# Performance work log

Measured on AMD Instinct MI355X. Metric: run time of the kernel, lower is better.

Reference implementation:

```python
import jax, jax.numpy as jnp
import numpy as np

B, P, L, M, L_EVAL = 8, 16, 256, 16, 2048
T_MAX = 100.0


def setup_inputs() -> dict:
    key = jax.random.key(0)
    k1, k2, k3, k4, k5 = jax.random.split(key, 5)
    # sorted event times per path (Hawkes event streams are ordered)
    event_times = jnp.sort(jax.random.uniform(k1, (B, P, L), dtype=jnp.float32) * T_MAX, axis=-1)
    # parameters are assumed already positive (post-softplus) -> uniform [0,1)
    mu = jax.random.uniform(k2, (B, M, P, L), dtype=jnp.float32)
    alpha = jax.random.uniform(k3, (B, M, P, L), dtype=jnp.float32)
    beta = jax.random.uniform(k4, (B, M, P, L), dtype=jnp.float32)
    query_times = jax.random.uniform(k5, (B, P, L_EVAL), dtype=jnp.float32) * T_MAX
    return {"query_times": query_times, "event_times": event_times,
            "mu": mu, "alpha": alpha, "beta": beta}


def reference(query_times, event_times, mu, alpha, beta):
    # query_times: [B,P,Le]; event_times: [B,P,L]; mu/alpha/beta: [B,M,P,L]
    b, m, p, l = mu.shape
    le = query_times.shape[-1]
    # index of latest event strictly before each query time (mask + max, as original)
    past_mask = event_times[:, :, None, :] < query_times[:, :, :, None]  # [B,P,Le,L]
    idx = jnp.arange(l, dtype=jnp.int32)
    last_idx = jnp.max(jnp.where(past_mask, idx, -1), axis=-1)            # [B,P,Le]
    ci = jnp.clip(last_idx, 0, None)
    gi = jnp.broadcast_to(ci[:, None, :, :], (b, m, p, le))
    mu_last = jnp.take_along_axis(mu, gi, axis=3)
    alpha_last = jnp.take_along_axis(alpha, gi, axis=3)
    beta_last = jnp.take_along_axis(beta, gi, axis=3)
    t_last = jnp.take_along_axis(event_times, ci, axis=2)                 # [B,P,Le]
    t_last = jnp.where(last_idx == -1, jnp.zeros_like(t_last), t_last)
    delta_t = (query_times - t_last)[:, None, :, :]                       # [B,1,P,Le]
    base = mu_last + (alpha_last - mu_last) * jnp.exp(-beta_last * delta_t)
    return jax.nn.softplus(base)                                          # [B,M,P,Le]
```

## Files before the change

### kernel.cpp

```cpp
#include <hip/hip_runtime.h>

#define BB  8
#define PP  16
#define LL  256
#define MM  16
#define LE  2048
#define THREADS 512
#define TILE THREADS

__device__ __forceinline__ void acc4(const float4 v, const float q, int& cin, float& tl)
{
    bool c;
    c = (v.x < q); cin += c; tl = c ? fmaxf(tl, v.x) : tl;
    c = (v.y < q); cin += c; tl = c ? fmaxf(tl, v.y) : tl;
    c = (v.z < q); cin += c; tl = c ? fmaxf(tl, v.z) : tl;
    c = (v.w < q); cin += c; tl = c ? fmaxf(tl, v.w) : tl;
}

__global__ __launch_bounds__(THREADS, 4) void hawkes_intensity_kernel(
    const float* __restrict__ qt,
    const float* __restrict__ ev,
    const float* __restrict__ mu,
    const float* __restrict__ alpha,
    const float* __restrict__ beta,
    float* __restrict__ out)
{
    __shared__ float2 pma_s[MM * LL];
    __shared__ float  pnb_s[MM * LL];
    __shared__ __align__(16) float ev_s[LL];

    const int tiles_per_bp = LE / TILE;
    const int bp   = blockIdx.x / tiles_per_bp;
    const int tile = blockIdx.x % tiles_per_bp;
    const int b = bp / PP;
    const int p = bp % PP;
    const int t = threadIdx.x;

    const int le = tile * TILE + t;
    const float q = qt[bp * LE + le];

    if (t < LL) ev_s[t] = ev[bp * LL + t];

    #pragma unroll
    for (int i = t; i < MM * LL; i += THREADS) {
        const int m = i >> 8;
        const int l = i & (LL - 1);
        const int g = ((b * MM + m) * PP + p) * LL + l;
        const float mm = mu[g];
        const float aa = alpha[g];
        const float bb = beta[g];
        pma_s[i] = make_float2(mm, aa - mm);
        pnb_s[i] = -bb;
    }
    __syncthreads();

    int F = 0;
    float tl = 0.0f;
    #pragma unroll
    for (int j = 0; j < 16; ++j) {
        const float r = ev_s[j * 16 + 15];
        const bool c = (r < q);
        F += c;
        tl = c ? fmaxf(tl, r) : tl;
    }
    const int Fc = (F < 16) ? F : 15;

    const float4* ev4 = (const float4*)ev_s;
    const float4 w0 = ev4[Fc * 4 + 0];
    const float4 w1 = ev4[Fc * 4 + 1];
    const float4 w2 = ev4[Fc * 4 + 2];
    const float4 w3 = ev4[Fc * 4 + 3];
    int cin = 0;
    acc4(w0, q, cin, tl);
    acc4(w1, q, cin, tl);
    acc4(w2, q, cin, tl);
    acc4(w3, q, cin, tl);

    const int cnt = Fc * 16 + cin;
    const int ci  = (cnt > 0) ? (cnt - 1) : 0;
    const float dt = q - tl;

    int o = (b * MM * PP + p) * LE + le;
    #pragma unroll
    for (int m = 0; m < MM; ++m) {
        const float2 pm = pma_s[(m << 8) | ci];
        const float  nb = pnb_s[(m << 8) | ci];
        const float  e  = __expf(nb * dt);
        const float  base = fmaf(pm.y, e, pm.x);
        out[o] = __logf(1.0f + __expf(base));
        o += PP * LE;
    }
}

extern "C" void kernel_launch(void* const* d_in, const int* in_sizes, int n_in,
                              void* d_out, int out_size, void* d_ws, size_t ws_size,
                              hipStream_t stream) {
    const float* qt    = (const float*)d_in[0];
    const float* ev    = (const float*)d_in[1];
    const float* mu    = (const float*)d_in[2];
    const float* alpha = (const float*)d_in[3];
    const float* beta  = (const float*)d_in[4];
    float* out = (float*)d_out;

    const int nblocks = (BB * PP) * (LE / TILE);
    hawkes_intensity_kernel<<<nblocks, THREADS, 0, stream>>>(qt, ev, mu, alpha, beta, out);
}
```

Measured before the change: 78.32 us.

## Split work by mark groups instead of query tiles to cut redundant parameter loads

The grid now covers (b,p) pairs times groups of two marks, so each block loads only two marks' worth of mu/alpha/beta into shared memory and handles all 2048 queries, four per thread. Before, every query tile reloaded all 16 marks' parameters, which duplicated global reads four times over. The cost is that the event search for each query now repeats across the 8 mark groups. The change also vectorises the parameter loads with float4, swizzles the block index, and raises the launch-bounds occupancy hint.

```diff
diff --git a/kernel.cpp b/kernel.cpp
--- a/kernel.cpp
+++ b/kernel.cpp
@@ -5,8 +5,10 @@
 #define LL  256
 #define MM  16
 #define LE  2048
+#define MG  2
+#define NMG (MM/MG)
 #define THREADS 512
-#define TILE THREADS
+#define QPT (LE/THREADS)
 
 __device__ __forceinline__ void acc4(const float4 v, const float q, int& cin, float& tl)
 {
@@ -17,7 +19,7 @@
     c = (v.w < q); cin += c; tl = c ? fmaxf(tl, v.w) : tl;
 }
 
-__global__ __launch_bounds__(THREADS, 4) void hawkes_intensity_kernel(
+__global__ __launch_bounds__(THREADS, 6) void hawkes_intensity_kernel(
     const float* __restrict__ qt,
     const float* __restrict__ ev,
     const float* __restrict__ mu,
@@ -25,70 +27,88 @@
     const float* __restrict__ beta,
     float* __restrict__ out)
 {
-    __shared__ float2 pma_s[MM * LL];
-    __shared__ float  pnb_s[MM * LL];
+    __shared__ float2 pma_s[MG * LL];
+    __shared__ float  pnb_s[MG * LL];
     __shared__ __align__(16) float ev_s[LL];
 
-    const int tiles_per_bp = LE / TILE;
-    const int bp   = blockIdx.x / tiles_per_bp;
-    const int tile = blockIdx.x % tiles_per_bp;
+    const int lid = (blockIdx.x & 7) * (BB * PP * NMG / 8) + (blockIdx.x >> 3);
+    const int bp  = lid >> 3;
+    const int mg  = lid & (NMG - 1);
     const int b = bp / PP;
     const int p = bp % PP;
     const int t = threadIdx.x;
 
-    const int le = tile * TILE + t;
-    const float q = qt[bp * LE + le];
+    const float* qrow = qt + bp * LE;
+    float qv[QPT];
+    #pragma unroll
+    for (int k = 0; k < QPT; ++k) qv[k] = qrow[k * THREADS + t];
 
-    if (t < LL) ev_s[t] = ev[bp * LL + t];
+    if (t >= 256) ev_s[t - 256] = ev[bp * LL + (t - 256)];
 
-    #pragma unroll
-    for (int i = t; i < MM * LL; i += THREADS) {
-        const int m = i >> 8;
-        const int l = i & (LL - 1);
-        const int g = ((b * MM + m) * PP + p) * LL + l;
-        const float mm = mu[g];
-        const float aa = alpha[g];
-        const float bb = beta[g];
-        pma_s[i] = make_float2(mm, aa - mm);
-        pnb_s[i] = -bb;
+    if (t < (MG * LL / 4)) {
+        const float4* mu4 = (const float4*)mu;
+        const float4* al4 = (const float4*)alpha;
+        const float4* be4 = (const float4*)beta;
+        const int m  = t >> 6;
+        const int l4 = t & 63;
+        const int g  = ((b * MM + mg * MG + m) * PP + p) * (LL / 4) + l4;
+        const float4 mv = mu4[g];
+        const float4 av = al4[g];
+        const float4 bv = be4[g];
+        const float ma[4] = {mv.x, mv.y, mv.z, mv.w};
+        const float aa[4] = {av.x, av.y, av.z, av.w};
+        const float ba[4] = {bv.x, bv.y, bv.z, bv.w};
+        #pragma unroll
+        for (int j = 0; j < 4; ++j) {
+            const int l = (l4 << 2) | j;
+            pma_s[(m << 8) | l] = make_float2(ma[j], aa[j] - ma[j]);
+            pnb_s[(m << 8) | l] = -ba[j];
+        }
     }
     __syncthreads();
 
-    int F = 0;
-    float tl = 0.0f;
+    const float4* ev4 = (const float4*)ev_s;
+
     #pragma unroll
-    for (int j = 0; j < 16; ++j) {
-        const float r = ev_s[j * 16 + 15];
-        const bool c = (r < q);
-        F += c;
-        tl = c ? fmaxf(tl, r) : tl;
-    }
-    const int Fc = (F < 16) ? F : 15;
+    for (int k = 0; k < QPT; ++k) {
+        const int le = k * THREADS + t;
+        const float q = qv[k];
 
-    const float4* ev4 = (const float4*)ev_s;
-    const float4 w0 = ev4[Fc * 4 + 0];
-    const float4 w1 = ev4[Fc * 4 + 1];
-    const float4 w2 = ev4[Fc * 4 + 2];
-    const float4 w3 = ev4[Fc * 4 + 3];
-    int cin = 0;
-    acc4(w0, q, cin, tl);
-    acc4(w1, q, cin, tl);
-    acc4(w2, q, cin, tl);
-    acc4(w3, q, cin, tl);
+        int F = 0;
+        float tl = 0.0f;
+        #pragma unroll
+        for (int j = 0; j < 16; ++j) {
+            const float r = ev_s[j * 16 + 15];
+            const bool c = (r < q);
+            F += c;
+            tl = c ? fmaxf(tl, r) : tl;
+        }
+        const int Fc = (F < 16) ? F : 15;
 
-    const int cnt = Fc * 16 + cin;
-    const int ci  = (cnt > 0) ? (cnt - 1) : 0;
-    const float dt = q - tl;
+        const float4 w0 = ev4[Fc * 4 + 0];
+        const float4 w1 = ev4[Fc * 4 + 1];
+        const float4 w2 = ev4[Fc * 4 + 2];
+        const float4 w3 = ev4[Fc * 4 + 3];
+        int cin = 0;
+        acc4(w0, q, cin, tl);
+        acc4(w1, q, cin, tl);
+        acc4(w2, q, cin, tl);
+        acc4(w3, q, cin, tl);
 
-    int o = (b * MM * PP + p) * LE + le;
-    #pragma unroll
-    for (int m = 0; m < MM; ++m) {
-        const float2 pm = pma_s[(m << 8) | ci];
-        const float  nb = pnb_s[(m << 8) | ci];
-        const float  e  = __expf(nb * dt);
-        const float  base = fmaf(pm.y, e, pm.x);
-        out[o] = __logf(1.0f + __expf(base));
-        o += PP * LE;
+        const int cnt = Fc * 16 + cin;
+        const int ci  = (cnt > 0) ? (cnt - 1) : 0;
+        const float dt = q - tl;
+
+        int o = ((b * MM + mg * MG) * PP + p) * LE + le;
+        #pragma unroll
+        for (int m = 0; m < MG; ++m) {
+            const float2 pm = pma_s[(m << 8) | ci];
+            const float  nb = pnb_s[(m << 8) | ci];
+            const float  e  = __expf(nb * dt);
+            const float  base = fmaf(pm.y, e, pm.x);
+            out[o] = __logf(1.0f + __expf(base));
+            o += PP * LE;
+        }
     }
 }
 
@@ -102,6 +122,6 @@
     const float* beta  = (const float*)d_in[4];
     float* out = (float*)d_out;
 
-    const int nblocks = (BB * PP) * (LE / TILE);
+    const int nblocks = BB * PP * NMG;
     hawkes_intensity_kernel<<<nblocks, THREADS, 0, stream>>>(qt, ev, mu, alpha, beta, out);
 }
```

After: 83.53 us. 6.7% more time.
